# Performance work log

Measured on AMD Instinct MI355X. Metric: run time of the kernel, lower is better.

## Reference

```python
import jax, jax.numpy as jnp
import numpy as np

V, D, H, L, T_MAX = 50257, 1024, 16, 12, 256
HS = D // H
B, T = 8, 256


def setup_inputs() -> dict:
    key = jax.random.key(0)
    ks = jax.random.split(key, 24)
    s = 0.02
    inp = {
        'idx': jax.random.randint(ks[0], (B, T), 0, V),
        'targets': jax.random.randint(ks[1], (B, T), 0, V),
        'tok_emb': jax.random.normal(ks[2], (V, D), jnp.float32) * s,
        'pos_emb': jax.random.normal(ks[3], (T_MAX, D), jnp.float32) * s,
        'Wq': jax.random.normal(ks[4], (L, H, D, HS), jnp.float32) / np.sqrt(D),
        'Wk': jax.random.normal(ks[5], (L, H, D, HS), jnp.float32) / np.sqrt(D),
        'Wv': jax.random.normal(ks[6], (L, H, D, HS), jnp.float32) / np.sqrt(D),
        'ln1_g': jnp.ones((L, D), jnp.float32),
        'ln1_b': jnp.zeros((L, D), jnp.float32),
        'ln2_g': jnp.ones((L, D), jnp.float32),
        'ln2_b': jnp.zeros((L, D), jnp.float32),
        'fc1_w': jax.random.normal(ks[7], (L, D, 4 * D), jnp.float32) / np.sqrt(D),
        'fc1_b': jnp.zeros((L, 4 * D), jnp.float32),
        'fc2_w': jax.random.normal(ks[8], (L, 4 * D, D), jnp.float32) / np.sqrt(4 * D),
        'fc2_b': jnp.zeros((L, D), jnp.float32),
        'lnf_g': jnp.ones((D,), jnp.float32),
        'lnf_b': jnp.zeros((D,), jnp.float32),
        'lm_w': jax.random.normal(ks[9], (D, V), jnp.float32) / np.sqrt(D),
        'lm_b': jnp.zeros((V,), jnp.float32),
    }
    return inp


def _layernorm(x, g, b, eps=1e-5):
    mu = jnp.mean(x, axis=-1, keepdims=True)
    var = jnp.var(x, axis=-1, keepdims=True)
    return (x - mu) * jax.lax.rsqrt(var + eps) * g + b


def reference(idx, targets, tok_emb, pos_emb, Wq, Wk, Wv, ln1_g, ln1_b, ln2_g, ln2_b,
              fc1_w, fc1_b, fc2_w, fc2_b, lnf_g, lnf_b, lm_w, lm_b):
    Bc, Tc = idx.shape
    x = tok_emb[idx] + pos_emb[:Tc]  # [B,T,D]
    causal = jnp.tril(jnp.ones((Tc, Tc), bool))
    scale = 1.0 / np.sqrt(HS)
    for l in range(L):
        h = _layernorm(x, ln1_g[l], ln1_b[l])
        q = jnp.einsum('btd,hds->bhts', h, Wq[l])
        k = jnp.einsum('btd,hds->bhts', h, Wk[l])
        v = jnp.einsum('btd,hds->bhts', h, Wv[l])
        scores = jnp.einsum('bhts,bhus->bhtu', q, k) * scale
        scores = jnp.where(causal, scores, -jnp.inf)
        attn = jax.nn.softmax(scores, axis=-1)
        o = jnp.einsum('bhtu,bhus->bhts', attn, v)  # [B,H,T,hs]
        o = o.transpose(0, 2, 1, 3).reshape(Bc, Tc, D)  # concat heads
        x = x + o  # no output projection in original
        h = _layernorm(x, ln2_g[l], ln2_b[l])
        ff = jax.nn.relu(h @ fc1_w[l] + fc1_b[l]) @ fc2_w[l] + fc2_b[l]
        x = x + ff
    x = _layernorm(x, lnf_g, lnf_b)
    logits = x @ lm_w + lm_b  # [B,T,V]
    logp = jax.nn.log_softmax(logits, axis=-1)
    nll = -jnp.take_along_axis(logp, targets[..., None], axis=-1)[..., 0]
    loss = jnp.mean(nll)
    return logits, loss
```

## Files before the change

kernel.cpp:

```cpp
#include <hip/hip_runtime.h>

#define T_SEQ 256
#define DMODEL 1024
#define NHEAD 16
#define HSZ 64
#define NLAYER 12
#define VOCAB 50257
#define NPAD 50304
#define FF 4096
#define MROWS 2048

using short8 = __attribute__((ext_vector_type(8))) short;
using f32x4  = __attribute__((ext_vector_type(4))) float;

__device__ __forceinline__ float bf2f(unsigned short u) {
    unsigned int x = ((unsigned int)u) << 16;
    return __builtin_bit_cast(float, x);
}
__device__ __forceinline__ unsigned short f2bf(float f) {
    unsigned int u = __builtin_bit_cast(unsigned int, f);
    unsigned int r = (u + 0x7fffu + ((u >> 16) & 1u)) >> 16;
    return (unsigned short)r;
}
__device__ __forceinline__ void async_copy16(const void* g, void* l) {
    __builtin_amdgcn_global_load_lds(
        (const __attribute__((address_space(1))) unsigned int*)g,
        (__attribute__((address_space(3))) unsigned int*)l, 16, 0, 0);
}

__device__ __forceinline__ void ln_tail(
    float4 v, const float* __restrict__ g, const float* __restrict__ b,
    int row, int tid, unsigned short* __restrict__ out)
{
    float s  = v.x + v.y + v.z + v.w;
    float ss = v.x * v.x + v.y * v.y + v.z * v.z + v.w * v.w;
    for (int o = 32; o > 0; o >>= 1) {
        s  += __shfl_down(s, o);
        ss += __shfl_down(ss, o);
    }
    __shared__ float ps[4], pss[4];
    int wave = tid >> 6, lane = tid & 63;
    if (lane == 0) { ps[wave] = s; pss[wave] = ss; }
    __syncthreads();
    float st  = ps[0] + ps[1] + ps[2] + ps[3];
    float sst = pss[0] + pss[1] + pss[2] + pss[3];
    float mu  = st * (1.0f / DMODEL);
    float var = sst * (1.0f / DMODEL) - mu * mu;
    float rstd = rsqrtf(var + 1e-5f);
    float4 gv = ((const float4*)g)[tid];
    float4 bv = ((const float4*)b)[tid];
    ushort4 o4;
    o4.x = f2bf((v.x - mu) * rstd * gv.x + bv.x);
    o4.y = f2bf((v.y - mu) * rstd * gv.y + bv.y);
    o4.z = f2bf((v.z - mu) * rstd * gv.z + bv.z);
    o4.w = f2bf((v.w - mu) * rstd * gv.w + bv.w);
    ((ushort4*)out)[(size_t)row * (DMODEL / 4) + tid] = o4;
}

__global__ __launch_bounds__(256) void embed_ln_kernel(
    const int* __restrict__ idx, const float* __restrict__ tok,
    const float* __restrict__ pos, const float* __restrict__ g,
    const float* __restrict__ b, float* __restrict__ x,
    unsigned short* __restrict__ h)
{
    int row = blockIdx.x, tid = threadIdx.x;
    int t = row & (T_SEQ - 1);
    int token = idx[row];
    float4 a = ((const float4*)(tok + (size_t)token * DMODEL))[tid];
    float4 p = ((const float4*)(pos + (size_t)t * DMODEL))[tid];
    float4 v;
    v.x = a.x + p.x; v.y = a.y + p.y; v.z = a.z + p.z; v.w = a.w + p.w;
    ((float4*)(x + (size_t)row * DMODEL))[tid] = v;
    ln_tail(v, g, b, row, tid, h);
}

__global__ __launch_bounds__(256) void ln_kernel(
    const float* __restrict__ x, const float* __restrict__ g,
    const float* __restrict__ b, unsigned short* __restrict__ out)
{
    int row = blockIdx.x, tid = threadIdx.x;
    float4 v = ((const float4*)(x + (size_t)row * DMODEL))[tid];
    ln_tail(v, g, b, row, tid, out);
}

__global__ __launch_bounds__(256) void fc2_merge_ln_kernel(
    const float* __restrict__ part, const float* __restrict__ bias,
    const float* __restrict__ g, const float* __restrict__ b,
    float* __restrict__ x, unsigned short* __restrict__ h)
{
    int row = blockIdx.x, tid = threadIdx.x;
    size_t o = (size_t)row * (DMODEL / 4) + tid;
    float4 p0 = ((const float4*)part)[o];
    float4 p1 = ((const float4*)part)[o + MROWS * (DMODEL / 4)];
    float4 bv = ((const float4*)bias)[tid];
    float4 v = ((float4*)x)[o];
    v.x += p0.x + p1.x + bv.x;
    v.y += p0.y + p1.y + bv.y;
    v.z += p0.z + p1.z + bv.z;
    v.w += p0.w + p1.w + bv.w;
    ((float4*)x)[o] = v;
    ln_tail(v, g, b, row, tid, h);
}

__global__ __launch_bounds__(256) void wtranspose_kernel(
    const float* __restrict__ in, unsigned short* __restrict__ out,
    int R, int C, int Cout, long in_l, long out_l)
{
    int lyr = blockIdx.z;
    in  += (size_t)lyr * in_l;
    out += (size_t)lyr * out_l;
    __shared__ float tile[32][33];
    int tx = threadIdx.x & 31, ty = threadIdx.x >> 5;
    int c0 = blockIdx.x * 32, r0 = blockIdx.y * 32;
    #pragma unroll
    for (int i = 0; i < 4; i++) {
        int r = r0 + ty + i * 8, c = c0 + tx;
        tile[ty + i * 8][tx] = (c < C) ? in[(size_t)r * C + c] : 0.f;
    }
    __syncthreads();
    int wrl = (threadIdx.x & 15) * 2;
    int wcl = threadIdx.x >> 4;
    #pragma unroll
    for (int i = 0; i < 2; i++) {
        int c = c0 + wcl + i * 16, r = r0 + wrl;
        if (c < Cout) {
            ushort2 w;
            w.x = f2bf(tile[wrl][wcl + i * 16]);
            w.y = f2bf(tile[wrl + 1][wcl + i * 16]);
            *(ushort2*)(out + (size_t)c * R + r) = w;
        }
    }
}

__global__ __launch_bounds__(256) void qkvpack_kernel(
    const float* __restrict__ Wq, const float* __restrict__ Wk,
    const float* __restrict__ Wv, unsigned short* __restrict__ out,
    long w_l, long out_l)
{
    int z = blockIdx.z;
    int lyr = z / 48, r48 = z % 48;
    int seg = r48 >> 4, hh = r48 & 15;
    const float* W = (seg == 0 ? Wq : seg == 1 ? Wk : Wv)
                     + (size_t)lyr * w_l + (size_t)hh * DMODEL * HSZ;
    unsigned short* o = out + (size_t)lyr * out_l
                      + (size_t)(seg * 1024 + hh * 64) * DMODEL;
    __shared__ float tile[32][33];
    int tx = threadIdx.x & 31, ty = threadIdx.x >> 5;
    int d0 = blockIdx.x * 32, s0 = blockIdx.y * 32;
    #pragma unroll
    for (int i = 0; i < 4; i++)
        tile[ty + i * 8][tx] = W[(size_t)(d0 + ty + i * 8) * HSZ + s0 + tx];
    __syncthreads();
    int wdl = (threadIdx.x & 15) * 2;
    int wsl = threadIdx.x >> 4;
    #pragma unroll
    for (int i = 0; i < 2; i++) {
        int s = s0 + wsl + i * 16, d = d0 + wdl;
        ushort2 w;
        w.x = f2bf(tile[wdl][wsl + i * 16]);
        w.y = f2bf(tile[wdl + 1][wsl + i * 16]);
        *(ushort2*)(o + (size_t)s * DMODEL + d) = w;
    }
}

template<int MF, int WAVES, bool QKV, bool RELU, bool RES, bool CBF16>
__device__ __forceinline__ void gemm_core(
    const unsigned short* __restrict__ A, int lda,
    const unsigned short* __restrict__ Bt, int ldb,
    const float* __restrict__ bias,
    void* __restrict__ Cv, int ldc,
    const float* __restrict__ res, int ldr,
    int N, int K,
    unsigned short* __restrict__ vtout)
{
    constexpr int BM = (WAVES / 2) * MF * 16;
    constexpr int BJ = 16 / WAVES;
    __shared__ __align__(16) char As[BM * 128];
    __shared__ __align__(16) char Bs[128 * 128];
    int tid = threadIdx.x;
    int wave = tid >> 6, lane = tid & 63;
    int wr = wave >> 1, wc = wave & 1;
    int m0 = blockIdx.x * BM, n0 = blockIdx.y * 128;

    f32x4 acc[MF][4];
    #pragma unroll
    for (int m = 0; m < MF; m++)
        #pragma unroll
        for (int n = 0; n < 4; n++)
            acc[m][n] = (f32x4){0.f, 0.f, 0.f, 0.f};

    int ksw = (((lane & 7) ^ (lane >> 3)) << 4);
    int KT = K >> 6;
    for (int kt = 0; kt < KT; kt++) {
        int k0 = kt << 6;
        __syncthreads();
        #pragma unroll
        for (int j = 0; j < MF; j++) {
            int row = (wave * MF + j) * 8 + (lane >> 3);
            const char* src = (const char*)A + ((size_t)(m0 + row) * lda + k0) * 2 + ksw;
            async_copy16(src, As + (wave * MF + j) * 1024);
        }
        #pragma unroll
        for (int j = 0; j < BJ; j++) {
            int nrow = (wave * BJ + j) * 8 + (lane >> 3);
            const char* src = (const char*)Bt + ((size_t)(n0 + nrow) * ldb + k0) * 2 + ksw;
            async_copy16(src, Bs + (wave * BJ + j) * 1024);
        }
        __syncthreads();
        #pragma unroll
        for (int ks = 0; ks < 2; ks++) {
            int kb = ks * 64 + ((lane >> 4) << 4);
            short8 a[MF], b[4];
            #pragma unroll
            for (int m = 0; m < MF; m++) {
                int r = wr * (MF * 16) + m * 16 + (lane & 15);
                a[m] = *(const short8*)(const void*)(As + r * 128 + (kb ^ ((r & 7) << 4)));
            }
            #pragma unroll
            for (int n = 0; n < 4; n++) {
                int c = wc * 64 + n * 16 + (lane & 15);
                b[n] = *(const short8*)(const void*)(Bs + c * 128 + (kb ^ ((c & 7) << 4)));
            }
            #pragma unroll
            for (int m = 0; m < MF; m++)
                #pragma unroll
                for (int n = 0; n < 4; n++)
                    acc[m][n] = __builtin_amdgcn_mfma_f32_16x16x32_bf16(a[m], b[n], acc[m][n], 0, 0, 0);
        }
    }
    #pragma unroll
    for (int m = 0; m < MF; m++) {
        int rowb = m0 + wr * (MF * 16) + m * 16 + ((lane >> 4) << 2);
        #pragma unroll
        for (int n = 0; n < 4; n++) {
            int col = n0 + wc * 64 + n * 16 + (lane & 15);
            if (col < N) {
                float bi = bias ? bias[col] : 0.f;
                #pragma unroll
                for (int r2 = 0; r2 < 4; r2++) {
                    float v = acc[m][n][r2] + bi;
                    if (RELU) v = fmaxf(v, 0.f);
                    int row = rowb + r2;
                    if (RES) v += res[(size_t)row * ldr + col];
                    if (QKV && col >= 2048) {
                        int hh = (col - 2048) >> 6, sdim = (col - 2048) & 63;
                        int bb = row >> 8, tt = row & 255;
                        vtout[((((size_t)bb * NHEAD + hh) * HSZ + sdim) * T_SEQ) + tt] = f2bf(v);
                    } else if (CBF16) {
                        ((unsigned short*)Cv)[(size_t)row * ldc + col] = f2bf(v);
                    } else {
                        ((float*)Cv)[(size_t)row * ldc + col] = v;
                    }
                }
            }
        }
    }
}

__global__ __launch_bounds__(256) void gemm_qkv(
    const unsigned short* __restrict__ A, const unsigned short* __restrict__ Bt,
    unsigned short* __restrict__ C, unsigned short* __restrict__ vtout)
{
    gemm_core<4, 4, true, false, false, true>(
        A, DMODEL, Bt, DMODEL, nullptr, C, 3072, nullptr, 0, 3072, DMODEL, vtout);
}

__global__ __launch_bounds__(256) void gemm_fc1(
    const unsigned short* __restrict__ A, const unsigned short* __restrict__ Bt,
    const float* __restrict__ bias, unsigned short* __restrict__ C)
{
    gemm_core<4, 4, false, true, false, true>(
        A, DMODEL, Bt, DMODEL, bias, C, FF, nullptr, 0, FF, DMODEL, nullptr);
}

__global__ __launch_bounds__(256) void gemm_fc2(
    const unsigned short* __restrict__ A, const unsigned short* __restrict__ Bt,
    float* __restrict__ part)
{
    int z = blockIdx.z;
    gemm_core<2, 4, false, false, false, false>(
        A + z * 2048, FF, Bt + z * 2048, FF, nullptr,
        part + (size_t)z * MROWS * DMODEL, DMODEL, nullptr, 0,
        DMODEL, 2048, nullptr);
}

__global__ __launch_bounds__(512) void gemm_lm(
    const unsigned short* __restrict__ A, const unsigned short* __restrict__ Bt,
    const float* __restrict__ bias, float* __restrict__ C)
{
    gemm_core<4, 8, false, false, false, false>(
        A, DMODEL, Bt, DMODEL, bias, C, VOCAB, nullptr, 0, VOCAB, DMODEL, nullptr);
}

__global__ __launch_bounds__(256) void attn_fused_kernel(
    const unsigned short* __restrict__ qkv, const unsigned short* __restrict__ vt,
    float* __restrict__ x)
{
    int qt = blockIdx.x, hh = blockIdx.y, b = blockIdx.z;
    int tid = threadIdx.x;
    int wave = tid >> 6, lane = tid & 63;
    int g = lane >> 4, q = lane & 15;

    __shared__ __align__(16) char Kb[4][8192];
    __shared__ __align__(16) char Vb[4][8192];
    __shared__ __align__(16) char Plds[4][2048];

    int qrow = b * T_SEQ + qt * 64 + wave * 16 + q;
    const char* qp = (const char*)qkv + ((size_t)qrow * 3072 + hh * HSZ) * 2;
    short8 qreg[2];
    qreg[0] = *(const short8*)(const void*)(qp + (g << 4));
    qreg[1] = *(const short8*)(const void*)(qp + 64 + (g << 4));

    char* Pw = Plds[wave];

    f32x4 oacc[4];
    #pragma unroll
    for (int f = 0; f < 4; f++) oacc[f] = (f32x4){0.f, 0.f, 0.f, 0.f};
    float m_run = -1e30f, l_run = 0.f;

    int srow = wave * 8 + (lane >> 3);
    int sbyte = ((lane & 7) << 4) ^ ((srow & 7) << 4);

    for (int kt = 0; kt <= qt; kt++) {
        #pragma unroll
        for (int c = 0; c < 2; c++) {
            int row = c * 32 + srow;
            const char* src = (const char*)qkv +
                ((size_t)(b * T_SEQ + kt * 64 + row) * 3072 + 1024 + hh * HSZ) * 2 + sbyte;
            async_copy16(src, Kb[kt] + c * 4096 + wave * 1024);
        }
        #pragma unroll
        for (int c = 0; c < 2; c++) {
            int row = c * 32 + srow;
            const char* src = (const char*)vt +
                (((size_t)(b * NHEAD + hh) * HSZ + row) * T_SEQ + kt * 64) * 2 + sbyte;
            async_copy16(src, Vb[kt] + c * 4096 + wave * 1024);
        }
    }
    __syncthreads();

    for (int kt = 0; kt <= qt; kt++) {
        f32x4 sacc[4];
        #pragma unroll
        for (int f = 0; f < 4; f++) sacc[f] = (f32x4){0.f, 0.f, 0.f, 0.f};
        #pragma unroll
        for (int ks = 0; ks < 2; ks++) {
            int kb = ks * 64 + (g << 4);
            #pragma unroll
            for (int f = 0; f < 4; f++) {
                int u = f * 16 + q;
                short8 kf = *(const short8*)(const void*)(Kb[kt] + u * 128 + (kb ^ ((u & 7) << 4)));
                sacc[f] = __builtin_amdgcn_mfma_f32_16x16x32_bf16(kf, qreg[ks], sacc[f], 0, 0, 0);
            }
        }
        float sv[4][4];
        #pragma unroll
        for (int f = 0; f < 4; f++)
            #pragma unroll
            for (int r = 0; r < 4; r++) {
                float v = sacc[f][r] * 0.125f;
                if (kt == qt) {
                    int u_loc = f * 16 + g * 4 + r;
                    if (u_loc > wave * 16 + q) v = -1e30f;
                }
                sv[f][r] = v;
            }
        float pm = -1e30f;
        #pragma unroll
        for (int f = 0; f < 4; f++)
            #pragma unroll
            for (int r = 0; r < 4; r++) pm = fmaxf(pm, sv[f][r]);
        pm = fmaxf(pm, __shfl_xor(pm, 16));
        pm = fmaxf(pm, __shfl_xor(pm, 32));
        float mnew = fmaxf(m_run, pm);
        float corr = __expf(m_run - mnew);
        float p[4][4];
        float ls = 0.f;
        #pragma unroll
        for (int f = 0; f < 4; f++)
            #pragma unroll
            for (int r = 0; r < 4; r++) {
                p[f][r] = __expf(sv[f][r] - mnew);
                ls += p[f][r];
            }
        ls += __shfl_xor(ls, 16);
        ls += __shfl_xor(ls, 32);
        l_run = l_run * corr + ls;
        m_run = mnew;
        #pragma unroll
        for (int r = 0; r < 4; r++) {
            float cr = __shfl(corr, (lane & 48) | (g * 4 + r));
            #pragma unroll
            for (int f = 0; f < 4; f++) oacc[f][r] *= cr;
        }
        #pragma unroll
        for (int f = 0; f < 4; f++)
            #pragma unroll
            for (int rp = 0; rp < 2; rp++) {
                int ue = f * 16 + g * 4 + rp * 2;
                unsigned int pk = (unsigned int)f2bf(p[f][rp * 2])
                                | ((unsigned int)f2bf(p[f][rp * 2 + 1]) << 16);
                *(unsigned int*)(void*)(Pw + q * 128 + ((ue * 2) ^ ((q & 7) << 4))) = pk;
            }
        #pragma unroll
        for (int ks = 0; ks < 2; ks++) {
            int kb = ks * 64 + (g << 4);
            short8 pa = *(const short8*)(const void*)(Pw + q * 128 + (kb ^ ((q & 7) << 4)));
            #pragma unroll
            for (int f = 0; f < 4; f++) {
                int s = f * 16 + q;
                short8 vf = *(const short8*)(const void*)(Vb[kt] + s * 128 + (kb ^ ((s & 7) << 4)));
                oacc[f] = __builtin_amdgcn_mfma_f32_16x16x32_bf16(pa, vf, oacc[f], 0, 0, 0);
            }
        }
    }
    float inv = 1.0f / l_run;
    #pragma unroll
    for (int r = 0; r < 4; r++) {
        float ir = __shfl(inv, (lane & 48) | (g * 4 + r));
        int row_g = b * T_SEQ + qt * 64 + wave * 16 + g * 4 + r;
        #pragma unroll
        for (int f = 0; f < 4; f++) {
            size_t xi = (size_t)row_g * DMODEL + hh * HSZ + f * 16 + q;
            x[xi] += oacc[f][r] * ir;
        }
    }
}

__global__ __launch_bounds__(256) void loss1_kernel(
    const float* __restrict__ logits, const int* __restrict__ targets,
    float* __restrict__ nll)
{
    int r = blockIdx.x, tid = threadIdx.x;
    const float* row = logits + (size_t)r * VOCAB;
    const float4* row4 = (const float4*)row;
    float m = -3.4e38f, s = 0.f;
    for (int v = tid; v < VOCAB / 4; v += 256) {
        float4 x4 = row4[v];
        float lm = fmaxf(fmaxf(x4.x, x4.y), fmaxf(x4.z, x4.w));
        float nm = fmaxf(m, lm);
        s = s * __expf(m - nm) + __expf(x4.x - nm) + __expf(x4.y - nm)
          + __expf(x4.z - nm) + __expf(x4.w - nm);
        m = nm;
    }
    if (tid == 0) {
        float xv = row[VOCAB - 1];
        float nm = fmaxf(m, xv);
        s = s * __expf(m - nm) + __expf(xv - nm);
        m = nm;
    }
    __shared__ float ms[256], ssh[256];
    ms[tid] = m; ssh[tid] = s;
    __syncthreads();
    for (int o = 128; o > 0; o >>= 1) {
        if (tid < o) {
            float m1 = ms[tid], s1 = ssh[tid];
            float m2 = ms[tid + o], s2 = ssh[tid + o];
            float nm = fmaxf(m1, m2);
            ssh[tid] = s1 * __expf(m1 - nm) + s2 * __expf(m2 - nm);
            ms[tid] = nm;
        }
        __syncthreads();
    }
    if (tid == 0) nll[r] = logf(ssh[0]) + ms[0] - row[targets[r]];
}

__global__ __launch_bounds__(256) void loss2_kernel(
    const float* __restrict__ nll, float* __restrict__ out)
{
    int tid = threadIdx.x;
    float s = 0.f;
    for (int i = tid; i < MROWS; i += 256) s += nll[i];
    __shared__ float red[256];
    red[tid] = s;
    __syncthreads();
    for (int o = 128; o > 0; o >>= 1) {
        if (tid < o) red[tid] += red[tid + o];
        __syncthreads();
    }
    if (tid == 0) out[0] = red[0] * (1.0f / MROWS);
}

extern "C" void kernel_launch(void* const* d_in, const int* in_sizes, int n_in,
                              void* d_out, int out_size, void* d_ws, size_t ws_size,
                              hipStream_t stream)
{
    const int*   idx  = (const int*)d_in[0];
    const int*   tgt  = (const int*)d_in[1];
    const float* tok  = (const float*)d_in[2];
    const float* pos  = (const float*)d_in[3];
    const float* Wq   = (const float*)d_in[4];
    const float* Wk   = (const float*)d_in[5];
    const float* Wv   = (const float*)d_in[6];
    const float* ln1g = (const float*)d_in[7];
    const float* ln1b = (const float*)d_in[8];
    const float* ln2g = (const float*)d_in[9];
    const float* ln2b = (const float*)d_in[10];
    const float* fc1w = (const float*)d_in[11];
    const float* fc1b = (const float*)d_in[12];
    const float* fc2w = (const float*)d_in[13];
    const float* fc2b = (const float*)d_in[14];
    const float* lnfg = (const float*)d_in[15];
    const float* lnfb = (const float*)d_in[16];
    const float* lmw  = (const float*)d_in[17];
    const float* lmb  = (const float*)d_in[18];

    char* ws = (char*)d_ws;
    float*          x    = (float*)(ws + 0);
    unsigned short* h    = (unsigned short*)(ws + 8388608);
    unsigned short* qkv  = (unsigned short*)(ws + 12582912);
    unsigned short* vt   = (unsigned short*)(ws + 25165824);
    unsigned short* mid  = (unsigned short*)(ws + 29360128);
    float*          nll  = (float*)(ws + 46137344);
    float*          fc2p = (float*)(ws + 46145536);
    unsigned short* lmwt = (unsigned short*)(ws + 62922752);
    const size_t UP_NEED = 442769408ull;
    bool upfront = (ws_size >= UP_NEED);
    unsigned short* qkvt = (unsigned short*)(ws + 165945344);
    unsigned short* fc1t, * fc2t;
    long qkvt_l, fc1t_l, fc2t_l;
    if (upfront) {
        fc1t = (unsigned short*)(ws + 241442816);
        fc2t = (unsigned short*)(ws + 342106112);
        qkvt_l = 3072 * 1024; fc1t_l = (long)FF * 1024; fc2t_l = (long)1024 * FF;
    } else {
        fc1t = (unsigned short*)(ws + 172236800);
        fc2t = (unsigned short*)(ws + 180625408);
        qkvt_l = 0; fc1t_l = 0; fc2t_l = 0;
    }
    float* logits = (float*)d_out;
    float* lossp  = logits + (size_t)MROWS * VOCAB;

    const long WQKV_L = (long)NHEAD * DMODEL * HSZ;
    if (upfront) {
        qkvpack_kernel<<<dim3(32, 2, 48 * NLAYER), 256, 0, stream>>>(
            Wq, Wk, Wv, qkvt, WQKV_L, qkvt_l);
        wtranspose_kernel<<<dim3(128, 32, NLAYER), 256, 0, stream>>>(
            fc1w, fc1t, DMODEL, FF, FF, (long)DMODEL * FF, fc1t_l);
        wtranspose_kernel<<<dim3(32, 128, NLAYER), 256, 0, stream>>>(
            fc2w, fc2t, FF, DMODEL, DMODEL, (long)FF * DMODEL, fc2t_l);
    }
    wtranspose_kernel<<<dim3(1572, 32, 1), 256, 0, stream>>>(
        lmw, lmwt, DMODEL, VOCAB, NPAD, 0, 0);

    embed_ln_kernel<<<MROWS, 256, 0, stream>>>(idx, tok, pos, ln1g, ln1b, x, h);

    for (int l = 0; l < NLAYER; l++) {
        unsigned short* qkvt_p = qkvt + (size_t)l * qkvt_l;
        unsigned short* fc1t_p = fc1t + (size_t)l * fc1t_l;
        unsigned short* fc2t_p = fc2t + (size_t)l * fc2t_l;
        if (!upfront) {
            qkvpack_kernel<<<dim3(32, 2, 48), 256, 0, stream>>>(
                Wq + (size_t)l * WQKV_L, Wk + (size_t)l * WQKV_L,
                Wv + (size_t)l * WQKV_L, qkvt, WQKV_L, 0);
            wtranspose_kernel<<<dim3(128, 32, 1), 256, 0, stream>>>(
                fc1w + (size_t)l * DMODEL * FF, fc1t, DMODEL, FF, FF, 0, 0);
            wtranspose_kernel<<<dim3(32, 128, 1), 256, 0, stream>>>(
                fc2w + (size_t)l * FF * DMODEL, fc2t, FF, DMODEL, DMODEL, 0, 0);
        }
        gemm_qkv<<<dim3(16, 24), 256, 0, stream>>>(h, qkvt_p, qkv, vt);
        attn_fused_kernel<<<dim3(4, NHEAD, 8), 256, 0, stream>>>(qkv, vt, x);
        ln_kernel<<<MROWS, 256, 0, stream>>>(x, ln2g + l * DMODEL, ln2b + l * DMODEL, h);
        gemm_fc1<<<dim3(16, 32), 256, 0, stream>>>(h, fc1t_p, fc1b + (size_t)l * FF, mid);
        gemm_fc2<<<dim3(32, 8, 2), 256, 0, stream>>>(mid, fc2t_p, fc2p);
        const float* ng = (l < NLAYER - 1) ? ln1g + (l + 1) * DMODEL : lnfg;
        const float* nb = (l < NLAYER - 1) ? ln1b + (l + 1) * DMODEL : lnfb;
        fc2_merge_ln_kernel<<<MROWS, 256, 0, stream>>>(
            fc2p, fc2b + (size_t)l * DMODEL, ng, nb, x, h);
    }

    gemm_lm<<<dim3(8, 393), 512, 0, stream>>>(h, lmwt, lmb, logits);

    loss1_kernel<<<MROWS, 256, 0, stream>>>(logits, tgt, nll);
    loss2_kernel<<<1, 256, 0, stream>>>(nll, lossp);
}
```

Baseline: 2.120 ms.

## Vectorize weight transposes with 64x64 tiles and widen fc1 GEMM tiles

The fp32-to-bf16 weight transpose and QKV pack kernels move from 32x32 tiles to 64x64 tiles. They read global memory with float4 loads and write 16-byte bf16 vectors, which cuts load/store instruction count and improves coalescing. The GEMM core gains a WCOLS parameter so the wave grid can be shaped independently of MF. fc1 now runs 8 waves in a 2x4 layout with 128x256 block tiles, raising B reuse per block in exchange for fewer blocks (256) and more LDS per block. The lm_head padding columns are now written from zero-filled tiles instead of being bounds-checked against NPAD.

```diff
diff --git a/kernel.cpp b/kernel.cpp
--- a/kernel.cpp
+++ b/kernel.cpp
@@ -102,37 +102,48 @@
     ln_tail(v, g, b, row, tid, h);
 }
 
-__global__ __launch_bounds__(256) void wtranspose_kernel(
+__global__ __launch_bounds__(256) void wtranspose64_kernel(
     const float* __restrict__ in, unsigned short* __restrict__ out,
-    int R, int C, int Cout, long in_l, long out_l)
+    int R, int C, long in_l, long out_l)
 {
     int lyr = blockIdx.z;
     in  += (size_t)lyr * in_l;
     out += (size_t)lyr * out_l;
-    __shared__ float tile[32][33];
-    int tx = threadIdx.x & 31, ty = threadIdx.x >> 5;
-    int c0 = blockIdx.x * 32, r0 = blockIdx.y * 32;
+    __shared__ float tile[64][65];
+    int tx = threadIdx.x & 15, ty = threadIdx.x >> 4;
+    int c0 = blockIdx.x * 64, r0 = blockIdx.y * 64;
     #pragma unroll
     for (int i = 0; i < 4; i++) {
-        int r = r0 + ty + i * 8, c = c0 + tx;
-        tile[ty + i * 8][tx] = (c < C) ? in[(size_t)r * C + c] : 0.f;
+        int r = ty + i * 16;
+        int c = tx * 4;
+        int gc = c0 + c;
+        const float* src = in + (size_t)(r0 + r) * C + gc;
+        float4 v;
+        if (gc + 3 < C) {
+            v = *(const float4*)src;
+        } else {
+            v.x = (gc     < C) ? src[0] : 0.f;
+            v.y = (gc + 1 < C) ? src[1] : 0.f;
+            v.z = (gc + 2 < C) ? src[2] : 0.f;
+            v.w = (gc + 3 < C) ? src[3] : 0.f;
+        }
+        tile[r][c] = v.x; tile[r][c + 1] = v.y;
+        tile[r][c + 2] = v.z; tile[r][c + 3] = v.w;
     }
     __syncthreads();
-    int wrl = (threadIdx.x & 15) * 2;
-    int wcl = threadIdx.x >> 4;
+    int sr = (threadIdx.x & 7) * 8;
+    int scb = threadIdx.x >> 3;
     #pragma unroll
     for (int i = 0; i < 2; i++) {
-        int c = c0 + wcl + i * 16, r = r0 + wrl;
-        if (c < Cout) {
-            ushort2 w;
-            w.x = f2bf(tile[wrl][wcl + i * 16]);
-            w.y = f2bf(tile[wrl + 1][wcl + i * 16]);
-            *(ushort2*)(out + (size_t)c * R + r) = w;
-        }
-    }
-}
-
-__global__ __launch_bounds__(256) void qkvpack_kernel(
+        int c = scb + i * 32;
+        unsigned short w[8];
+        #pragma unroll
+        for (int j = 0; j < 8; j++) w[j] = f2bf(tile[sr + j][c]);
+        *(short8*)(void*)(out + (size_t)(c0 + c) * R + r0 + sr) = *(short8*)(void*)w;
+    }
+}
+
+__global__ __launch_bounds__(256) void qkvpack64_kernel(
     const float* __restrict__ Wq, const float* __restrict__ Wk,
     const float* __restrict__ Wv, unsigned short* __restrict__ out,
     long w_l, long out_l)
@@ -144,26 +155,30 @@
                      + (size_t)lyr * w_l + (size_t)hh * DMODEL * HSZ;
     unsigned short* o = out + (size_t)lyr * out_l
                       + (size_t)(seg * 1024 + hh * 64) * DMODEL;
-    __shared__ float tile[32][33];
-    int tx = threadIdx.x & 31, ty = threadIdx.x >> 5;
-    int d0 = blockIdx.x * 32, s0 = blockIdx.y * 32;
-    #pragma unroll
-    for (int i = 0; i < 4; i++)
-        tile[ty + i * 8][tx] = W[(size_t)(d0 + ty + i * 8) * HSZ + s0 + tx];
+    __shared__ float tile[64][65];
+    int tx = threadIdx.x & 15, ty = threadIdx.x >> 4;
+    int d0 = blockIdx.x * 64;
+    #pragma unroll
+    for (int i = 0; i < 4; i++) {
+        int d = ty + i * 16;
+        float4 v = *(const float4*)(W + (size_t)(d0 + d) * HSZ + tx * 4);
+        tile[d][tx * 4] = v.x; tile[d][tx * 4 + 1] = v.y;
+        tile[d][tx * 4 + 2] = v.z; tile[d][tx * 4 + 3] = v.w;
+    }
     __syncthreads();
-    int wdl = (threadIdx.x & 15) * 2;
-    int wsl = threadIdx.x >> 4;
+    int db = (threadIdx.x & 7) * 8;
+    int sb = threadIdx.x >> 3;
     #pragma unroll
     for (int i = 0; i < 2; i++) {
-        int s = s0 + wsl + i * 16, d = d0 + wdl;
-        ushort2 w;
-        w.x = f2bf(tile[wdl][wsl + i * 16]);
-        w.y = f2bf(tile[wdl + 1][wsl + i * 16]);
-        *(ushort2*)(o + (size_t)s * DMODEL + d) = w;
-    }
-}
-
-template<int MF, int WAVES, bool QKV, bool RELU, bool RES, bool CBF16>
+        int s = sb + i * 32;
+        unsigned short w[8];
+        #pragma unroll
+        for (int j = 0; j < 8; j++) w[j] = f2bf(tile[db + j][s]);
+        *(short8*)(void*)(o + (size_t)s * DMODEL + d0 + db) = *(short8*)(void*)w;
+    }
+}
+
+template<int MF, int WAVES, int WCOLS, bool QKV, bool RELU, bool RES, bool CBF16>
 __device__ __forceinline__ void gemm_core(
     const unsigned short* __restrict__ A, int lda,
     const unsigned short* __restrict__ Bt, int ldb,
@@ -173,14 +188,16 @@
     int N, int K,
     unsigned short* __restrict__ vtout)
 {
-    constexpr int BM = (WAVES / 2) * MF * 16;
-    constexpr int BJ = 16 / WAVES;
+    constexpr int BM = MF * 16 * (WAVES / WCOLS);
+    constexpr int BN = 64 * WCOLS;
+    constexpr int AJ = (BM * 8) / (WAVES * 64);
+    constexpr int BJ = (BN * 8) / (WAVES * 64);
     __shared__ __align__(16) char As[BM * 128];
-    __shared__ __align__(16) char Bs[128 * 128];
+    __shared__ __align__(16) char Bs[BN * 128];
     int tid = threadIdx.x;
     int wave = tid >> 6, lane = tid & 63;
-    int wr = wave >> 1, wc = wave & 1;
-    int m0 = blockIdx.x * BM, n0 = blockIdx.y * 128;
+    int wr = wave / WCOLS, wc = wave % WCOLS;
+    int m0 = blockIdx.x * BM, n0 = blockIdx.y * BN;
 
     f32x4 acc[MF][4];
     #pragma unroll
@@ -195,10 +212,10 @@
         int k0 = kt << 6;
         __syncthreads();
         #pragma unroll
-        for (int j = 0; j < MF; j++) {
-            int row = (wave * MF + j) * 8 + (lane >> 3);
+        for (int j = 0; j < AJ; j++) {
+            int row = (wave * AJ + j) * 8 + (lane >> 3);
             const char* src = (const char*)A + ((size_t)(m0 + row) * lda + k0) * 2 + ksw;
-            async_copy16(src, As + (wave * MF + j) * 1024);
+            async_copy16(src, As + (wave * AJ + j) * 1024);
         }
         #pragma unroll
         for (int j = 0; j < BJ; j++) {
@@ -261,15 +278,15 @@
     const unsigned short* __restrict__ A, const unsigned short* __restrict__ Bt,
     unsigned short* __restrict__ C, unsigned short* __restrict__ vtout)
 {
-    gemm_core<4, 4, true, false, false, true>(
+    gemm_core<4, 4, 2, true, false, false, true>(
         A, DMODEL, Bt, DMODEL, nullptr, C, 3072, nullptr, 0, 3072, DMODEL, vtout);
 }
 
-__global__ __launch_bounds__(256) void gemm_fc1(
+__global__ __launch_bounds__(512) void gemm_fc1(
     const unsigned short* __restrict__ A, const unsigned short* __restrict__ Bt,
     const float* __restrict__ bias, unsigned short* __restrict__ C)
 {
-    gemm_core<4, 4, false, true, false, true>(
+    gemm_core<4, 8, 4, false, true, false, true>(
         A, DMODEL, Bt, DMODEL, bias, C, FF, nullptr, 0, FF, DMODEL, nullptr);
 }
 
@@ -278,7 +295,7 @@
     float* __restrict__ part)
 {
     int z = blockIdx.z;
-    gemm_core<2, 4, false, false, false, false>(
+    gemm_core<2, 4, 2, false, false, false, false>(
         A + z * 2048, FF, Bt + z * 2048, FF, nullptr,
         part + (size_t)z * MROWS * DMODEL, DMODEL, nullptr, 0,
         DMODEL, 2048, nullptr);
@@ -288,7 +305,7 @@
     const unsigned short* __restrict__ A, const unsigned short* __restrict__ Bt,
     const float* __restrict__ bias, float* __restrict__ C)
 {
-    gemm_core<4, 8, false, false, false, false>(
+    gemm_core<4, 8, 2, false, false, false, false>(
         A, DMODEL, Bt, DMODEL, bias, C, VOCAB, nullptr, 0, VOCAB, DMODEL, nullptr);
 }
 
@@ -533,15 +550,15 @@
 
     const long WQKV_L = (long)NHEAD * DMODEL * HSZ;
     if (upfront) {
-        qkvpack_kernel<<<dim3(32, 2, 48 * NLAYER), 256, 0, stream>>>(
+        qkvpack64_kernel<<<dim3(16, 1, 48 * NLAYER), 256, 0, stream>>>(
             Wq, Wk, Wv, qkvt, WQKV_L, qkvt_l);
-        wtranspose_kernel<<<dim3(128, 32, NLAYER), 256, 0, stream>>>(
-            fc1w, fc1t, DMODEL, FF, FF, (long)DMODEL * FF, fc1t_l);
-        wtranspose_kernel<<<dim3(32, 128, NLAYER), 256, 0, stream>>>(
-            fc2w, fc2t, FF, DMODEL, DMODEL, (long)FF * DMODEL, fc2t_l);
-    }
-    wtranspose_kernel<<<dim3(1572, 32, 1), 256, 0, stream>>>(
-        lmw, lmwt, DMODEL, VOCAB, NPAD, 0, 0);
+        wtranspose64_kernel<<<dim3(64, 16, NLAYER), 256, 0, stream>>>(
+            fc1w, fc1t, DMODEL, FF, (long)DMODEL * FF, fc1t_l);
+        wtranspose64_kernel<<<dim3(16, 64, NLAYER), 256, 0, stream>>>(
+            fc2w, fc2t, FF, DMODEL, (long)FF * DMODEL, fc2t_l);
+    }
+    wtranspose64_kernel<<<dim3(786, 16, 1), 256, 0, stream>>>(
+        lmw, lmwt, DMODEL, VOCAB, 0, 0);
 
     embed_ln_kernel<<<MROWS, 256, 0, stream>>>(idx, tok, pos, ln1g, ln1b, x, h);
 
@@ -550,18 +567,18 @@
         unsigned short* fc1t_p = fc1t + (size_t)l * fc1t_l;
         unsigned short* fc2t_p = fc2t + (size_t)l * fc2t_l;
         if (!upfront) {
-            qkvpack_kernel<<<dim3(32, 2, 48), 256, 0, stream>>>(
+            qkvpack64_kernel<<<dim3(16, 1, 48), 256, 0, stream>>>(
                 Wq + (size_t)l * WQKV_L, Wk + (size_t)l * WQKV_L,
                 Wv + (size_t)l * WQKV_L, qkvt, WQKV_L, 0);
-            wtranspose_kernel<<<dim3(128, 32, 1), 256, 0, stream>>>(
-                fc1w + (size_t)l * DMODEL * FF, fc1t, DMODEL, FF, FF, 0, 0);
-            wtranspose_kernel<<<dim3(32, 128, 1), 256, 0, stream>>>(
-                fc2w + (size_t)l * FF * DMODEL, fc2t, FF, DMODEL, DMODEL, 0, 0);
+            wtranspose64_kernel<<<dim3(64, 16, 1), 256, 0, stream>>>(
+                fc1w + (size_t)l * DMODEL * FF, fc1t, DMODEL, FF, 0, 0);
+            wtranspose64_kernel<<<dim3(16, 64, 1), 256, 0, stream>>>(
+                fc2w + (size_t)l * FF * DMODEL, fc2t, FF, DMODEL, 0, 0);
         }
         gemm_qkv<<<dim3(16, 24), 256, 0, stream>>>(h, qkvt_p, qkv, vt);
         attn_fused_kernel<<<dim3(4, NHEAD, 8), 256, 0, stream>>>(qkv, vt, x);
         ln_kernel<<<MROWS, 256, 0, stream>>>(x, ln2g + l * DMODEL, ln2b + l * DMODEL, h);
-        gemm_fc1<<<dim3(16, 32), 256, 0, stream>>>(h, fc1t_p, fc1b + (size_t)l * FF, mid);
+        gemm_fc1<<<dim3(16, 16), 512, 0, stream>>>(h, fc1t_p, fc1b + (size_t)l * FF, mid);
         gemm_fc2<<<dim3(32, 8, 2), 256, 0, stream>>>(mid, fc2t_p, fc2p);
         const float* ng = (l < NLAYER - 1) ? ln1g + (l + 1) * DMODEL : lnfg;
         const float* nb = (l < NLAYER - 1) ? ln1b + (l + 1) * DMODEL : lnfb;
```

Result: no change. 2.143 ms (+1.1%).
